# Performance work log

Hardware: AMD Instinct MI355X
Metric: run time of the kernel (lower is better)

The kernel has to match this reference:

```python
import jax, jax.numpy as jnp
import numpy as np

N_ATOMS = 50000
D = 256            # atom_embedding_size == transformer_embedding_size
F, G, A = 4, 50000, 3
L = 2              # num_transformers
IN_DIM = 2 * D     # concat(gathered atoms, tiled clique state)


def setup_inputs() -> dict:
    key = jax.random.key(0)
    ks = jax.random.split(key, 6)
    scale = 1.0 / np.sqrt(IN_DIM)
    return {
        "x": jax.random.normal(ks[0], (1, N_ATOMS, D), dtype=jnp.float32),
        "grounding_indices": jax.random.randint(ks[1], (F, G, A), 0, N_ATOMS, dtype=jnp.int32),
        "first_gcs": jax.random.normal(ks[2], (F, G, D), dtype=jnp.float32),
        "W_M": jax.random.normal(ks[3], (L, F, IN_DIM, D), dtype=jnp.float32) * scale,
        "b_M": jnp.zeros((L, F, D), dtype=jnp.float32),
        "W_U": jax.random.normal(ks[4], (L, F, IN_DIM, D), dtype=jnp.float32) * scale,
        "b_U": jnp.zeros((L, F, D), dtype=jnp.float32),
    }


def reference(x, grounding_indices, first_gcs, W_M, b_M, W_U, b_U):
    # x: [1, N, D]; grounding_indices: [F, G, A]; first_gcs: [F, G, D]
    atom = x[0]                                   # [N, D]
    n_atoms = atom.shape[0]
    f, g, a = grounding_indices.shape
    emb = W_U.shape[-1]
    gcl = first_gcs                               # clique state [F, G, D]
    flat_idx = grounding_indices.reshape(-1)      # [F*G*A]
    for i in range(L):
        gathered = atom[grounding_indices]        # [F, G, A, D]
        tiled = jnp.broadcast_to(gcl[:, :, None, :], (f, g, a, gcl.shape[-1]))
        gc_fi = jnp.concatenate([gathered, tiled], axis=-1)   # [F, G, A, 2D]
        if i < L - 1:
            # message transform Mc + max over atoms in clique -> new clique state
            gc = jax.nn.relu(jnp.einsum('fgai,fio->fgao', gc_fi, W_M[i])
                             + b_M[i][:, None, None, :])
            gcl = jnp.max(gc, axis=2)             # [F, G, emb]
        # update transform Mn, then scatter-max back to atoms
        fi = jax.nn.relu(jnp.einsum('fgai,fio->fgao', gc_fi, W_U[i])
                         + b_U[i][:, None, None, :])          # [F, G, A, emb]
        atom = jnp.zeros((n_atoms, emb), fi.dtype).at[flat_idx].max(
            fi.reshape(-1, emb))
    return atom[None]                             # [1, N, emb]
```

## Files before the change

### kernel.cpp

```cpp
#include <hip/hip_runtime.h>
#include <stdint.h>

#define NA 50000
#define DD 256
#define NF 4
#define NG 50000
#define MM 150000
#define TOT 600000
#define NAP2 50048
#define NT2 391
#define KK 256

typedef __attribute__((ext_vector_type(8))) short s16x8;
typedef __attribute__((ext_vector_type(4))) float f32x4;

__device__ __forceinline__ unsigned short f2bf(float f) {
  union { float f; uint32_t u; } v; v.f = f;
  return (unsigned short)((v.u + 0x7FFFu + ((v.u >> 16) & 1u)) >> 16);
}
__device__ __forceinline__ float bf2f(unsigned short h) {
  union { uint32_t u; float f; } v; v.u = ((uint32_t)h) << 16; return v.f;
}
__device__ __forceinline__ void gld_lds16(const void* g, void* l) {
  __builtin_amdgcn_global_load_lds(
      (const __attribute__((address_space(1))) uint32_t*)g,
      (__attribute__((address_space(3))) uint32_t*)l, 16, 0, 0);
}

__global__ void cvt_tile(const float* __restrict__ src, unsigned short* __restrict__ dst) {
  int blk = blockIdx.x;
  int cp = blk & 1, kb = (blk >> 1) & 7, rem = blk >> 4;
  int tile = rem % NT2, b = rem / NT2;
  int cl = threadIdx.x >> 7, row = threadIdx.x & 127;
  int c = cp * 2 + cl;
  int grow = tile * 128 + row;
  union { unsigned short h[8]; uint4 u; } o;
  if (grow < NA) {
    const float* s = src + ((size_t)b * NA + grow) * 256 + kb * 32 + c * 8;
    float4 v0 = *(const float4*)s, v1 = *(const float4*)(s + 4);
    o.h[0]=f2bf(v0.x); o.h[1]=f2bf(v0.y); o.h[2]=f2bf(v0.z); o.h[3]=f2bf(v0.w);
    o.h[4]=f2bf(v1.x); o.h[5]=f2bf(v1.y); o.h[6]=f2bf(v1.z); o.h[7]=f2bf(v1.w);
  } else o.u = make_uint4(0, 0, 0, 0);
  *(uint4*)(dst + (size_t)b * NAP2 * 256 +
            ((size_t)(tile * 8 + kb) * 512 + c * 128 + row) * 8) = o.u;
}

__global__ void prep_w(const float* __restrict__ WM, const float* __restrict__ WU,
                       unsigned short* __restrict__ Wt) {
  int t = blockIdx.x * 256 + threadIdx.x;
  if (t >= 196608) return;
  const float* src;
  if (t < 131072) {
    int e = t & 65535;
    int f = e >> 14, nt = (e >> 13) & 1, r = e & 8191;
    int k = ((r >> 10) << 5) + (((r >> 8) & 3) << 3) + ((t >> 16) << 8);
    int n = r & 255;
    src = (nt ? WU : WM) + ((size_t)f * 512 + k) * 256 + n;
  } else {
    int e = t - 131072;
    int bot = e >> 15;
    e &= 32767;
    int f = e >> 13, r = e & 8191;
    int k = ((r >> 10) << 5) + (((r >> 8) & 3) << 3) + (bot << 8);
    int n = r & 255;
    src = WU + ((size_t)(NF + f) * 512 + k) * 256 + n;
  }
  union { unsigned short h[8]; uint4 u; } o;
#pragma unroll
  for (int e2 = 0; e2 < 8; ++e2) o.h[e2] = f2bf(src[(size_t)e2 * 256]);
  ((uint4*)Wt)[t] = o.u;
}

__global__ void sort_count(const int* __restrict__ gi, uint32_t* __restrict__ cnt) {
  int t = blockIdx.x * 256 + threadIdx.x;
  if (t < TOT) atomicAdd(&cnt[gi[t]], 1u);
}
__global__ void sort_scan(const uint32_t* __restrict__ cnt, uint32_t* __restrict__ off,
                          uint32_t* __restrict__ bump) {
  __shared__ uint32_t part[1024];
  const int t = threadIdx.x;
  const int CH = 49;
  int lo = t * CH, hi = lo + CH; if (hi > NA) hi = NA;
  uint32_t s = 0;
  for (int i = lo; i < hi; ++i) s += cnt[i];
  part[t] = s;
  __syncthreads();
  for (int d = 1; d < 1024; d <<= 1) {
    uint32_t v = (t >= d) ? part[t - d] : 0u;
    __syncthreads();
    part[t] += v;
    __syncthreads();
  }
  uint32_t run = (t == 0) ? 0u : part[t - 1];
  for (int i = lo; i < hi; ++i) { off[i] = run; bump[i] = run; run += cnt[i]; }
  if (t == 1023) off[NA] = part[1023];
}
__global__ void sort_fill(const int* __restrict__ gi, uint32_t* __restrict__ bump,
                          uint32_t* __restrict__ occList) {
  int t = blockIdx.x * 256 + threadIdx.x;
  if (t < TOT) { uint32_t r = atomicAdd(&bump[gi[t]], 1u); occList[r] = (uint32_t)t; }
}

template <int L>
__global__ __launch_bounds__(512, 1)
void pgemm(const unsigned short* __restrict__ Aatom,
           const unsigned short* __restrict__ Agcl,
           const unsigned short* __restrict__ Wt,
           unsigned short* __restrict__ Pa,
           unsigned short* __restrict__ Pg)
{
  constexpr int RW = (L == 0) ? 512 : 256;
  const int ch = blockIdx.x, w = blockIdx.y;
  int side, f, nt;
  if (L == 0) { side = w >> 3; f = (w >> 1) & 3; nt = w & 1; }
  else        { side = w >> 2; f = w & 3; nt = 0; }
  int tbase, tcnt;
  if (L == 0) { tbase = (ch < 7) ? ch * 25 : 175 + (ch - 7) * 24; tcnt = (ch < 7) ? 25 : 24; }
  else        { tbase = (ch < 7) ? ch * 13 : 91 + (ch - 7) * 12;  tcnt = (ch < 7) ? 13 : 12; }

  const size_t wslot = (L == 0) ? ((size_t)side * 65536 + (size_t)(f * 2 + nt) * 8192)
                                : ((size_t)131072 + (size_t)side * 32768 + (size_t)f * 8192);
  const unsigned short* Wm = Wt + wslot * 8;
  const unsigned short* Ab = side ? (Agcl + (size_t)f * NAP2 * 256) : Aatom;
  unsigned short* P = (side ? Pg : Pa) + (size_t)f * NAP2 * RW + nt * 256;

  const int tid = threadIdx.x, lane = tid & 63, wid = tid >> 6;
  const int wm = wid >> 2, wn = wid & 3;
  const int hi = lane >> 4, lo = lane & 15;

  __shared__ unsigned short Wl[65536];
  __shared__ unsigned short Ar[3][4096];

#pragma unroll
  for (int r = 0; r < 16; ++r)
    gld_lds16(Wm + ((size_t)(r * 8 + wid) * 64 + lane) * 8, &Wl[(r * 8 + wid) * 512]);

  const unsigned short* as = Ab + (size_t)tbase * 32768 + (size_t)(wid * 64 + lane) * 8;
  const int NS = tcnt * 8;

  f32x4 acc[4][4];
#pragma unroll
  for (int m = 0; m < 4; ++m)
#pragma unroll
    for (int n = 0; n < 4; ++n) acc[m][n] = (f32x4)0.f;

  gld_lds16(as, &Ar[0][wid * 512]);
  gld_lds16(as + 4096, &Ar[1][wid * 512]);

  int cur = 0;
  for (int tl = 0; tl < tcnt; ++tl) {
#pragma unroll
    for (int kb = 0; kb < 8; ++kb) {
      if (kb == 1 || kb == 2) {
        if (tl > 0) asm volatile("s_waitcnt vmcnt(17)" ::: "memory");
        else        asm volatile("s_waitcnt vmcnt(1)" ::: "memory");
      } else if (kb == 7) {
        if (tl == tcnt - 1) asm volatile("s_waitcnt vmcnt(0)" ::: "memory");
        else                asm volatile("s_waitcnt vmcnt(1)" ::: "memory");
      } else {
        asm volatile("s_waitcnt vmcnt(1)" ::: "memory");
      }
      __builtin_amdgcn_sched_barrier(0);
      __builtin_amdgcn_s_barrier();
      __builtin_amdgcn_sched_barrier(0);

      {
        const int s = tl * 8 + kb;
        if (s + 2 < NS) {
          int b2 = cur + 2; if (b2 >= 3) b2 -= 3;
          gld_lds16(as + (size_t)(s + 2) * 4096, &Ar[b2][wid * 512]);
        }
      }

      if (kb == 0 && tl > 0) {
        const size_t rb = (size_t)(tbase + tl - 1) * 128 + wm * 64;
#pragma unroll
        for (int m = 0; m < 4; ++m)
#pragma unroll
          for (int n = 0; n < 4; ++n) {
            union { unsigned short h[4]; uint2 u; } o;
#pragma unroll
            for (int r = 0; r < 4; ++r) { o.h[r] = f2bf(acc[m][n][r]); acc[m][n][r] = 0.f; }
            *(uint2*)&P[(rb + m * 16 + lo) * RW + wn * 64 + n * 16 + hi * 4] = o.u;
          }
      }

      const unsigned short* Abuf = Ar[cur];
      s16x8 bv[4], av[4];
#pragma unroll
      for (int n = 0; n < 4; ++n)
        bv[n] = *(const s16x8*)&Wl[(kb * 1024 + hi * 256 + wn * 64 + n * 16 + lo) * 8];
#pragma unroll
      for (int m = 0; m < 4; ++m)
        av[m] = *(const s16x8*)&Abuf[(hi * 128 + wm * 64 + m * 16 + lo) * 8];
#pragma unroll
      for (int m = 0; m < 4; ++m)
#pragma unroll
        for (int n = 0; n < 4; ++n)
          acc[m][n] = __builtin_amdgcn_mfma_f32_16x16x32_bf16(bv[n], av[m], acc[m][n], 0, 0, 0);

      ++cur; if (cur >= 3) cur = 0;
    }
  }
  {
    const size_t rb = (size_t)(tbase + tcnt - 1) * 128 + wm * 64;
#pragma unroll
    for (int m = 0; m < 4; ++m)
#pragma unroll
      for (int n = 0; n < 4; ++n) {
        union { unsigned short h[4]; uint2 u; } o;
#pragma unroll
        for (int r = 0; r < 4; ++r) o.h[r] = f2bf(acc[m][n][r]);
        *(uint2*)&P[(rb + m * 16 + lo) * RW + wn * 64 + n * 16 + hi * 4] = o.u;
      }
  }
}

__global__ __launch_bounds__(256)
void msg_combine(const unsigned short* __restrict__ Pa,
                 const unsigned short* __restrict__ Pg,
                 const int* __restrict__ gIdx,
                 const float* __restrict__ bM,
                 unsigned short* __restrict__ gclT1)
{
  const int grp = blockIdx.x * 8 + (threadIdx.x >> 5);
  const int cl = threadIdx.x & 31;
  const int f = grp / NAP2, g = grp - f * NAP2;
  const int tile = g >> 7, row = g & 127;
  const int kb = cl >> 2, c = cl & 3;
  unsigned short* dp = gclT1 + (size_t)f * NAP2 * 256 +
                       ((size_t)(tile * 8 + kb) * 512 + c * 128 + row) * 8;
  if (g >= NG) { *(uint4*)dp = make_uint4(0, 0, 0, 0); return; }
  const int cc = cl * 8;
  const int* ip = gIdx + (size_t)f * MM + g * 3;
  int i0 = ip[0], i1 = ip[1], i2 = ip[2];
  const unsigned short* PaF = Pa + (size_t)f * NAP2 * 512;
  union { unsigned short h[8]; uint4 u; } a0, a1, a2, pg, o;
  a0.u = *(const uint4*)(PaF + (size_t)i0 * 512 + cc);
  a1.u = *(const uint4*)(PaF + (size_t)i1 * 512 + cc);
  a2.u = *(const uint4*)(PaF + (size_t)i2 * 512 + cc);
  pg.u = *(const uint4*)(Pg + ((size_t)f * NAP2 + g) * 512 + cc);
  const float4 b0 = *(const float4*)(bM + f * 256 + cc);
  const float4 b1 = *(const float4*)(bM + f * 256 + cc + 4);
  const float bb[8] = {b0.x, b0.y, b0.z, b0.w, b1.x, b1.y, b1.z, b1.w};
#pragma unroll
  for (int j = 0; j < 8; ++j) {
    float m = fmaxf(fmaxf(bf2f(a0.h[j]), bf2f(a1.h[j])), bf2f(a2.h[j]));
    o.h[j] = f2bf(fmaxf(m + bf2f(pg.h[j]) + bb[j], 0.f));
  }
  *(uint4*)dp = o.u;
}

template <int L>
__global__ __launch_bounds__(256)
void upd_combine(const unsigned short* __restrict__ Pa,
                 const unsigned short* __restrict__ Pg,
                 const uint32_t* __restrict__ offA,
                 const uint32_t* __restrict__ occList,
                 const float* __restrict__ bU,
                 unsigned short* __restrict__ outT,
                 float* __restrict__ outF)
{
  constexpr int RW = (L == 0) ? 512 : 256;
  constexpr int CO = (L == 0) ? 256 : 0;
  const int a = blockIdx.x * 4 + (threadIdx.x >> 6);
  const int lane = threadIdx.x & 63;
  const int h = lane >> 5, cl = lane & 31;
  const int cc = cl * 8;
  if (L == 0 && a >= NA) {
    if (a < NAP2 && h == 0) {
      int tile = a >> 7, row = a & 127;
      *(uint4*)(outT + ((size_t)(tile * 8 + (cl >> 2)) * 512 + (cl & 3) * 128 + row) * 8) =
          make_uint4(0, 0, 0, 0);
    }
    return;
  }
  if (a >= NA) return;

  float pa0[8], pa1[8], pa2[8], pa3[8];
  {
    union { unsigned short s[8]; uint4 u; } v;
#define LOADPA(F, DST)                                                          \
    v.u = *(const uint4*)(Pa + ((size_t)(F) * NAP2 + a) * RW + CO + cc);        \
    { const float4 b0 = *(const float4*)(bU + (F) * 256 + cc);                  \
      const float4 b1 = *(const float4*)(bU + (F) * 256 + cc + 4);              \
      DST[0]=bf2f(v.s[0])+b0.x; DST[1]=bf2f(v.s[1])+b0.y;                       \
      DST[2]=bf2f(v.s[2])+b0.z; DST[3]=bf2f(v.s[3])+b0.w;                       \
      DST[4]=bf2f(v.s[4])+b1.x; DST[5]=bf2f(v.s[5])+b1.y;                       \
      DST[6]=bf2f(v.s[6])+b1.z; DST[7]=bf2f(v.s[7])+b1.w; }
    LOADPA(0, pa0) LOADPA(1, pa1) LOADPA(2, pa2) LOADPA(3, pa3)
#undef LOADPA
  }

  float zm[8] = {0.f, 0.f, 0.f, 0.f, 0.f, 0.f, 0.f, 0.f};
  const uint32_t s = offA[a], e = offA[a + 1];
  for (uint32_t base = s; base < e; base += 64) {
    int cnt = (int)(e - base); if (cnt > 64) cnt = 64;
    uint32_t tmine = (base + lane < e) ? occList[base + lane] : 0u;
    for (int k = 0; k < cnt; k += 2) {
      int src = k + h;
      uint32_t t = __shfl(tmine, src);
      if (src < cnt) {
        int f = (int)(t / (uint32_t)MM);
        int g = (int)((t - (uint32_t)f * MM) / 3u);
        union { unsigned short s[8]; uint4 u; } v;
        v.u = *(const uint4*)(Pg + ((size_t)f * NAP2 + g) * RW + CO + cc);
#pragma unroll
        for (int j = 0; j < 8; ++j) {
          float paf = (f == 0) ? pa0[j] : (f == 1) ? pa1[j] : (f == 2) ? pa2[j] : pa3[j];
          zm[j] = fmaxf(zm[j], paf + bf2f(v.s[j]));
        }
      }
    }
  }
#pragma unroll
  for (int j = 0; j < 8; ++j) zm[j] = fmaxf(zm[j], __shfl_xor(zm[j], 32));

  if (L == 0) {
    if (h == 0) {
      union { unsigned short s[8]; uint4 u; } o;
#pragma unroll
      for (int j = 0; j < 8; ++j) o.s[j] = f2bf(zm[j]);
      int tile = a >> 7, row = a & 127;
      *(uint4*)(outT + ((size_t)(tile * 8 + (cl >> 2)) * 512 + (cl & 3) * 128 + row) * 8) = o.u;
    }
  } else {
    float4 o;
    if (h == 0) { o.x = zm[0]; o.y = zm[1]; o.z = zm[2]; o.w = zm[3];
                  *(float4*)(outF + (size_t)a * 256 + cc) = o; }
    else        { o.x = zm[4]; o.y = zm[5]; o.z = zm[6]; o.w = zm[7];
                  *(float4*)(outF + (size_t)a * 256 + cc + 4) = o; }
  }
}

extern "C" void kernel_launch(void* const* d_in, const int* in_sizes, int n_in,
                              void* d_out, int out_size, void* d_ws, size_t ws_size,
                              hipStream_t stream) {
  const float* x  = (const float*)d_in[0];
  const int*   gi = (const int*)d_in[1];
  const float* fg = (const float*)d_in[2];
  const float* WM = (const float*)d_in[3];
  const float* bM = (const float*)d_in[4];
  const float* WU = (const float*)d_in[5];
  const float* bU = (const float*)d_in[6];
  float* out = (float*)d_out;

  char* ws = (char*)d_ws;
  size_t off_b = 0;
  auto alloc = [&](size_t b) { char* p = ws + off_b; off_b += (b + 255) & ~(size_t)255; return p; };
  unsigned short* atomT = (unsigned short*)alloc((size_t)NAP2 * 256 * 2);
  unsigned short* gclT  = (unsigned short*)alloc((size_t)NF * NAP2 * 256 * 2);
  unsigned short* P0a   = (unsigned short*)alloc((size_t)NF * NAP2 * 512 * 2);
  unsigned short* P0g   = (unsigned short*)alloc((size_t)NF * NAP2 * 512 * 2);
  unsigned short* Wt    = (unsigned short*)alloc((size_t)196608 * 16);
  uint32_t* cnt     = (uint32_t*)alloc((size_t)NA * 4);
  uint32_t* offA    = (uint32_t*)alloc((size_t)(NA + 1) * 4);
  uint32_t* bump    = (uint32_t*)alloc((size_t)NA * 4);
  uint32_t* occList = (uint32_t*)alloc((size_t)TOT * 4);

  unsigned short* P1a = P0a;
  unsigned short* P1g = P0a + (size_t)NF * NAP2 * 256;

  cvt_tile<<<NT2 * 16, 256, 0, stream>>>(x, atomT);
  cvt_tile<<<NF * NT2 * 16, 256, 0, stream>>>(fg, gclT);
  prep_w<<<768, 256, 0, stream>>>(WM, WU, Wt);
  hipMemsetAsync(cnt, 0, (size_t)NA * 4, stream);
  sort_count<<<(TOT + 255) / 256, 256, 0, stream>>>(gi, cnt);
  sort_scan<<<1, 1024, 0, stream>>>(cnt, offA, bump);
  sort_fill<<<(TOT + 255) / 256, 256, 0, stream>>>(gi, bump, occList);

  pgemm<0><<<dim3(16, 16), 512, 0, stream>>>(atomT, gclT, Wt, P0a, P0g);
  msg_combine<<<NF * NAP2 / 8, 256, 0, stream>>>(P0a, P0g, gi, bM, gclT);
  upd_combine<0><<<NAP2 / 4, 256, 0, stream>>>(P0a, P0g, offA, occList, bU, atomT, nullptr);

  pgemm<1><<<dim3(32, 8), 512, 0, stream>>>(atomT, gclT, Wt, P1a, P1g);
  upd_combine<1><<<(NA + 3) / 4, 256, 0, stream>>>(P1a, P1g, offA, occList, bU + 1024, nullptr, out);
}
```

Baseline: 1.006 ms.

## Deepen A-tile prefetch to four buffers and spread epilogue stores across k-steps

The GEMM main loop now keeps four LDS A buffers with three tiles in flight instead of three buffers with two. The bf16 epilogue stores of the previous output tile move into a second accumulator set and are written two fragments per k-step, instead of all at once at kb==0. The aim is to hide global-load latency and spread store traffic over the MFMA work. In exchange it doubles the accumulator registers and raises launch_bounds min-blocks to 2, which may cause spills or register pressure. The 128KB of weight LDS per block probably still limits occupancy to one block per CU.

```diff
diff --git a/kernel.cpp b/kernel.cpp
--- a/kernel.cpp
+++ b/kernel.cpp
@@ -102,7 +102,7 @@
 }
 
 template <int L>
-__global__ __launch_bounds__(512, 1)
+__global__ __launch_bounds__(512, 2)
 void pgemm(const unsigned short* __restrict__ Aatom,
            const unsigned short* __restrict__ Agcl,
            const unsigned short* __restrict__ Wt,
@@ -129,7 +129,7 @@
   const int hi = lane >> 4, lo = lane & 15;
 
   __shared__ unsigned short Wl[65536];
-  __shared__ unsigned short Ar[3][4096];
+  __shared__ unsigned short Ar[4][4096];
 
 #pragma unroll
   for (int r = 0; r < 16; ++r)
@@ -138,7 +138,7 @@
   const unsigned short* as = Ab + (size_t)tbase * 32768 + (size_t)(wid * 64 + lane) * 8;
   const int NS = tcnt * 8;
 
-  f32x4 acc[4][4];
+  f32x4 acc[4][4], accS[4][4];
 #pragma unroll
   for (int m = 0; m < 4; ++m)
 #pragma unroll
@@ -146,62 +146,78 @@
 
   gld_lds16(as, &Ar[0][wid * 512]);
   gld_lds16(as + 4096, &Ar[1][wid * 512]);
-
-  int cur = 0;
-  for (int tl = 0; tl < tcnt; ++tl) {
+  gld_lds16(as + 8192, &Ar[2][wid * 512]);
+
+#define MFMA_BODY(KB, S)                                                        \
+  {                                                                             \
+    const unsigned short* Abuf = Ar[(S) & 3];                                   \
+    s16x8 bv[4], av[4];                                                         \
+    _Pragma("unroll")                                                           \
+    for (int n = 0; n < 4; ++n)                                                 \
+      bv[n] = *(const s16x8*)&Wl[((KB) * 1024 + hi * 256 + wn * 64 + n * 16 + lo) * 8]; \
+    _Pragma("unroll")                                                           \
+    for (int m = 0; m < 4; ++m)                                                 \
+      av[m] = *(const s16x8*)&Abuf[(hi * 128 + wm * 64 + m * 16 + lo) * 8];     \
+    _Pragma("unroll")                                                           \
+    for (int m = 0; m < 4; ++m)                                                 \
+      _Pragma("unroll")                                                         \
+      for (int n = 0; n < 4; ++n)                                               \
+        acc[m][n] = __builtin_amdgcn_mfma_f32_16x16x32_bf16(bv[n], av[m], acc[m][n], 0, 0, 0); \
+  }
+
+#define WAITB(VM)                                                               \
+  asm volatile("s_waitcnt vmcnt(" #VM ")" ::: "memory");                        \
+  __builtin_amdgcn_sched_barrier(0);                                            \
+  __builtin_amdgcn_s_barrier();                                                 \
+  __builtin_amdgcn_sched_barrier(0);
+
+#pragma unroll
+  for (int kb = 0; kb < 8; ++kb) {
+    WAITB(2)
+    gld_lds16(as + (size_t)(kb + 3) * 4096, &Ar[(kb + 3) & 3][wid * 512]);
+    __builtin_amdgcn_sched_barrier(0);
+    MFMA_BODY(kb, kb)
+  }
+#pragma unroll
+  for (int m = 0; m < 4; ++m)
+#pragma unroll
+    for (int n = 0; n < 4; ++n) { accS[m][n] = acc[m][n]; acc[m][n] = (f32x4)0.f; }
+
+  for (int tl = 1; tl < tcnt; ++tl) {
+    const size_t rbPrev = (size_t)(tbase + tl - 1) * 128 + wm * 64;
 #pragma unroll
     for (int kb = 0; kb < 8; ++kb) {
-      if (kb == 1 || kb == 2) {
-        if (tl > 0) asm volatile("s_waitcnt vmcnt(17)" ::: "memory");
-        else        asm volatile("s_waitcnt vmcnt(1)" ::: "memory");
-      } else if (kb == 7) {
-        if (tl == tcnt - 1) asm volatile("s_waitcnt vmcnt(0)" ::: "memory");
-        else                asm volatile("s_waitcnt vmcnt(1)" ::: "memory");
-      } else {
-        asm volatile("s_waitcnt vmcnt(1)" ::: "memory");
+      const int s = tl * 8 + kb;
+      if (kb == 0)      { if (tl == 1) { WAITB(2) } else { WAITB(8) } }
+      else if (kb == 1) { if (tl == 1) { WAITB(4) } else { WAITB(8) } }
+      else if (kb == 2) { if (tl == 1) { WAITB(6) } else { WAITB(8) } }
+      else if (kb == 6) { if (tl == tcnt - 1) { WAITB(7) } else { WAITB(8) } }
+      else if (kb == 7) { if (tl == tcnt - 1) { WAITB(6) } else { WAITB(8) } }
+      else              { WAITB(8) }
+
+      if (s + 3 < NS)
+        gld_lds16(as + (size_t)(s + 3) * 4096, &Ar[(s + 3) & 3][wid * 512]);
+      __builtin_amdgcn_sched_barrier(0);
+
+#pragma unroll
+      for (int j = 0; j < 2; ++j) {
+        const int p = kb * 2 + j, m = p >> 2, n = p & 3;
+        union { unsigned short h[4]; uint2 u; } o;
+#pragma unroll
+        for (int r = 0; r < 4; ++r) o.h[r] = f2bf(accS[m][n][r]);
+        *(uint2*)&P[(rbPrev + m * 16 + lo) * RW + wn * 64 + n * 16 + hi * 4] = o.u;
       }
-      __builtin_amdgcn_sched_barrier(0);
-      __builtin_amdgcn_s_barrier();
-      __builtin_amdgcn_sched_barrier(0);
-
-      {
-        const int s = tl * 8 + kb;
-        if (s + 2 < NS) {
-          int b2 = cur + 2; if (b2 >= 3) b2 -= 3;
-          gld_lds16(as + (size_t)(s + 2) * 4096, &Ar[b2][wid * 512]);
-        }
-      }
-
-      if (kb == 0 && tl > 0) {
-        const size_t rb = (size_t)(tbase + tl - 1) * 128 + wm * 64;
-#pragma unroll
-        for (int m = 0; m < 4; ++m)
-#pragma unroll
-          for (int n = 0; n < 4; ++n) {
-            union { unsigned short h[4]; uint2 u; } o;
-#pragma unroll
-            for (int r = 0; r < 4; ++r) { o.h[r] = f2bf(acc[m][n][r]); acc[m][n][r] = 0.f; }
-            *(uint2*)&P[(rb + m * 16 + lo) * RW + wn * 64 + n * 16 + hi * 4] = o.u;
-          }
-      }
-
-      const unsigned short* Abuf = Ar[cur];
-      s16x8 bv[4], av[4];
-#pragma unroll
-      for (int n = 0; n < 4; ++n)
-        bv[n] = *(const s16x8*)&Wl[(kb * 1024 + hi * 256 + wn * 64 + n * 16 + lo) * 8];
+
+      MFMA_BODY(kb, s)
+    }
+    if (tl < tcnt - 1) {
 #pragma unroll
       for (int m = 0; m < 4; ++m)
-        av[m] = *(const s16x8*)&Abuf[(hi * 128 + wm * 64 + m * 16 + lo) * 8];
-#pragma unroll
-      for (int m = 0; m < 4; ++m)
-#pragma unroll
-        for (int n = 0; n < 4; ++n)
-          acc[m][n] = __builtin_amdgcn_mfma_f32_16x16x32_bf16(bv[n], av[m], acc[m][n], 0, 0, 0);
-
-      ++cur; if (cur >= 3) cur = 0;
-    }
-  }
+#pragma unroll
+        for (int n = 0; n < 4; ++n) { accS[m][n] = acc[m][n]; acc[m][n] = (f32x4)0.f; }
+    }
+  }
+
   {
     const size_t rb = (size_t)(tbase + tcnt - 1) * 128 + wm * 64;
 #pragma unroll
@@ -214,6 +230,8 @@
         *(uint2*)&P[(rb + m * 16 + lo) * RW + wn * 64 + n * 16 + hi * 4] = o.u;
       }
   }
+#undef MFMA_BODY
+#undef WAITB
 }
 
 __global__ __launch_bounds__(256)
```

Result: faster. 914.9 us (-9.0%).
